# Performance work log

Measured on AMD Instinct MI355X. Metric: run time of the kernel, lower is better.

Reference implementation:

```python
import jax, jax.numpy as jnp
import numpy as np

TEMP = 16.0  # sqrt(in_dim=256), module default when temperature=None
BN_EPS = 1e-5


def setup_inputs() -> dict:
    key = jax.random.key(0)
    ks = jax.random.split(key, 8)
    B, Cin, T, H, W = 8, 256, 8, 16, 16
    FF, Cout = 512, 256
    # small init scale keeps softmax logits in a sane range
    s = 0.02
    return {
        "x": jax.random.normal(ks[0], (B, Cin, T, H, W), jnp.float32),
        "Wk": jax.random.normal(ks[1], (FF, Cin), jnp.float32) * s,
        "Wq": jax.random.normal(ks[2], (FF, Cin), jnp.float32) * s,
        "Wv": jax.random.normal(ks[3], (FF, Cin), jnp.float32) * s,
        "Wout": jax.random.normal(ks[4], (Cout, FF), jnp.float32) * s,
        "bout": jax.random.normal(ks[5], (Cout,), jnp.float32) * s,
        "gamma": jnp.ones((Cout,), jnp.float32),
        "beta": jnp.zeros((Cout,), jnp.float32),
    }


def reference(x, Wk, Wq, Wv, Wout, bout, gamma, beta):
    B, Cin, T, H, W = x.shape
    N = T * H * W
    xf = x.reshape(B, Cin, N)                      # 1x1x1 conv == per-position matmul
    K = jnp.einsum('fc,bcn->bfn', Wk, xf)
    Q = jnp.einsum('fc,bcn->bfn', Wq, xf)
    V = jnp.einsum('fc,bcn->bfn', Wv, xf)
    KQ = jnp.einsum('bfi,bfj->bij', K, Q)          # [B, N, N] = K^T Q
    attn = jax.nn.softmax(KQ / TEMP, axis=2)
    # torch: sum(V[:, :, :, None] * attn[:, None], dim=3)
    #      = V[b,c,i] * sum_j attn[b,i,j]  (no need to materialize B x C x N x N)
    agg = V * jnp.sum(attn, axis=2)[:, None, :]    # [B, FF, N]
    o = jnp.einsum('of,bfn->bon', Wout, agg) + bout[None, :, None]
    o = jax.nn.relu(o).reshape(B, -1, T, H, W)
    y = x + o                                      # residual (in_dim == out_dim)
    # BatchNorm3d, training mode (fresh module): batch stats over (B, T, H, W)
    mean = jnp.mean(y, axis=(0, 2, 3, 4), keepdims=True)
    var = jnp.var(y, axis=(0, 2, 3, 4), keepdims=True)
    g = gamma[None, :, None, None, None]
    b = beta[None, :, None, None, None]
    return g * (y - mean) * jax.lax.rsqrt(var + BN_EPS) + b
```

## Files before the change

### kernel.cpp

```cpp
#include <hip/hip_runtime.h>

typedef __attribute__((ext_vector_type(8))) short short8;
typedef __attribute__((ext_vector_type(4))) float floatx4;

#define B_    8
#define CIN   256
#define NSP   2048
#define FF    512
#define COUT  256
#define NTOT  (B_*COUT*NSP)

__device__ __forceinline__ unsigned short f2bf(float f) {
  unsigned int u = __float_as_uint(f);
  u += 0x7fffu + ((u >> 16) & 1u);
  return (unsigned short)(u >> 16);
}

__global__ __launch_bounds__(256) void k1_prep(
    const float* __restrict__ x, const float* __restrict__ Wv,
    const float* __restrict__ Wout,
    unsigned short* __restrict__ Mb, unsigned short* __restrict__ XT,
    float* __restrict__ stats)
{
  __shared__ float lds[64 * 65];
  const int tid = threadIdx.x;
  const int bx  = blockIdx.x;

  if (bx < 32) {
    if (bx == 0) { stats[tid] = 0.f; stats[256 + tid] = 0.f; }
    const int rbase = bx * 8;
    #pragma unroll
    for (int i = 0; i < 16; ++i) {
      int idx = i * 256 + tid;
      lds[idx] = Wout[(size_t)rbase * 512 + idx];
    }
    __syncthreads();
    float acc[8] = {0.f,0.f,0.f,0.f,0.f,0.f,0.f,0.f};
    #pragma unroll 8
    for (int f = 0; f < 512; ++f) {
      float w = Wv[(size_t)f * 256 + tid];
      #pragma unroll
      for (int j = 0; j < 8; ++j) acc[j] += lds[j * 512 + f] * w;
    }
    #pragma unroll
    for (int j = 0; j < 8; ++j)
      Mb[(size_t)(rbase + j) * 256 + tid] = f2bf(acc[j]);
  } else {
    const int idx = bx - 32;
    const int b   = idx >> 7;
    const int rem = idx & 127;
    const int n0  = (rem & 31) * 64;
    const int c0  = (rem >> 5) * 64;
    const float* xb = x + (size_t)b * CIN * NSP;
    const int n_l = tid & 63;
    const int c_l0 = tid >> 6;
    #pragma unroll
    for (int p = 0; p < 16; ++p) {
      int c_l = c_l0 + p * 4;
      lds[c_l * 65 + n_l] = xb[(size_t)(c0 + c_l) * NSP + n0 + n_l];
    }
    __syncthreads();
    const int cp   = tid & 31;
    const int n_l2 = tid >> 5;
    unsigned int* XT32 = (unsigned int*)XT;
    #pragma unroll
    for (int p = 0; p < 8; ++p) {
      int nn = n_l2 + p * 8;
      unsigned short lo = f2bf(lds[(2 * cp)     * 65 + nn]);
      unsigned short hi = f2bf(lds[(2 * cp + 1) * 65 + nn]);
      XT32[((size_t)b * NSP + n0 + nn) * 128 + (c0 >> 1) + cp] =
          (unsigned int)lo | ((unsigned int)hi << 16);
    }
  }
}

__global__ __launch_bounds__(256) void k2_gemm(
    const float* __restrict__ x, const unsigned short* __restrict__ Mb,
    const unsigned short* __restrict__ XT, const float* __restrict__ bout,
    unsigned short* __restrict__ ybf, float* __restrict__ stats)
{
  __shared__ float ls[128], lq[128];
  const int tid  = threadIdx.x;
  const int lane = tid & 63;
  const int wave = tid >> 6;
  const int b    = blockIdx.z;
  const int ocb  = blockIdx.y * 128;
  const int nb   = blockIdx.x * 128;
  const int wocb = ocb + (wave & 1) * 64;
  const int wnb  = nb + (wave >> 1) * 64;
  const int m16  = lane & 15;
  const int q    = lane >> 4;

  if (tid < 128) { ls[tid] = 0.f; lq[tid] = 0.f; }

  floatx4 acc[4][4];
  #pragma unroll
  for (int i = 0; i < 4; ++i)
    #pragma unroll
    for (int j = 0; j < 4; ++j)
      acc[i][j] = (floatx4){0.f, 0.f, 0.f, 0.f};

  const unsigned short* Abase = Mb + (size_t)(wocb + m16) * 256 + q * 8;
  const unsigned short* Bbase = XT + ((size_t)b * NSP + wnb + m16) * 256 + q * 8;

  #pragma unroll
  for (int kk = 0; kk < 8; ++kk) {
    short8 av[4], bv[4];
    #pragma unroll
    for (int t = 0; t < 4; ++t) {
      av[t] = *(const short8*)(Abase + (size_t)t * 16 * 256 + kk * 32);
      bv[t] = *(const short8*)(Bbase + (size_t)t * 16 * 256 + kk * 32);
    }
    #pragma unroll
    for (int i = 0; i < 4; ++i)
      #pragma unroll
      for (int j = 0; j < 4; ++j)
        acc[i][j] = __builtin_amdgcn_mfma_f32_16x16x32_bf16(av[i], bv[j], acc[i][j], 0, 0, 0);
  }

  __syncthreads();

  #pragma unroll
  for (int ti = 0; ti < 4; ++ti) {
    #pragma unroll
    for (int r = 0; r < 4; ++r) {
      const int oc = wocb + ti * 16 + q * 4 + r;
      const float bo = bout[oc];
      float s = 0.f, s2 = 0.f;
      #pragma unroll
      for (int tj = 0; tj < 4; ++tj) {
        const int n = wnb + tj * 16 + m16;
        float o = acc[ti][tj][r] + bo;
        o = fmaxf(o, 0.f);
        const size_t gidx = ((size_t)(b * COUT + oc)) * NSP + n;
        float y = x[gidx] + o;
        ybf[gidx] = f2bf(y);
        s += y;
        s2 += y * y;
      }
      #pragma unroll
      for (int d = 1; d < 16; d <<= 1) {
        s  += __shfl_xor(s, d, 64);
        s2 += __shfl_xor(s2, d, 64);
      }
      if (m16 == 0) {
        atomicAdd(&ls[oc - ocb], s);
        atomicAdd(&lq[oc - ocb], s2);
      }
    }
  }
  __syncthreads();
  if (tid < 128) {
    atomicAdd(&stats[ocb + tid], ls[tid]);
    atomicAdd(&stats[256 + ocb + tid], lq[tid]);
  }
}

__global__ void k3_finalize(const float* __restrict__ stats,
                            const float* __restrict__ gamma,
                            const float* __restrict__ beta,
                            float* __restrict__ scsh)
{
  const int c = threadIdx.x;
  const float inv_n = 1.f / 16384.f;
  float m = stats[c] * inv_n;
  float v = stats[256 + c] * inv_n - m * m;
  float inv = rsqrtf(v + 1e-5f);
  float sc = gamma[c] * inv;
  scsh[c] = sc;
  scsh[256 + c] = beta[c] - m * sc;
}

__global__ __launch_bounds__(256) void k4_norm(
    const unsigned short* __restrict__ ybf, const float* __restrict__ scsh,
    float* __restrict__ out)
{
  const size_t i = ((size_t)blockIdx.x * 256 + threadIdx.x) * 8;
  const int c = (int)((i >> 11) & 255);
  const float sc = scsh[c], sh = scsh[256 + c];
  const uint4 raw = *(const uint4*)(ybf + i);
  float4 o0, o1;
  o0.x = __uint_as_float(raw.x << 16)         * sc + sh;
  o0.y = __uint_as_float(raw.x & 0xffff0000u) * sc + sh;
  o0.z = __uint_as_float(raw.y << 16)         * sc + sh;
  o0.w = __uint_as_float(raw.y & 0xffff0000u) * sc + sh;
  o1.x = __uint_as_float(raw.z << 16)         * sc + sh;
  o1.y = __uint_as_float(raw.z & 0xffff0000u) * sc + sh;
  o1.z = __uint_as_float(raw.w << 16)         * sc + sh;
  o1.w = __uint_as_float(raw.w & 0xffff0000u) * sc + sh;
  *(float4*)(out + i)     = o0;
  *(float4*)(out + i + 4) = o1;
}

extern "C" void kernel_launch(void* const* d_in, const int* in_sizes, int n_in,
                              void* d_out, int out_size, void* d_ws, size_t ws_size,
                              hipStream_t stream) {
  const float* x     = (const float*)d_in[0];
  const float* Wv    = (const float*)d_in[3];
  const float* Wout  = (const float*)d_in[4];
  const float* bout  = (const float*)d_in[5];
  const float* gamma = (const float*)d_in[6];
  const float* beta  = (const float*)d_in[7];
  float* out = (float*)d_out;

  char* w = (char*)d_ws;
  unsigned short* Mb = (unsigned short*)w;
  unsigned short* XT = (unsigned short*)(w + 131072);
  unsigned short* yb = (unsigned short*)(w + 131072 + 8388608);
  float* stats = (float*)(w + 131072 + 8388608 + 8388608);
  float* scsh  = stats + 512;

  hipLaunchKernelGGL(k1_prep, dim3(32 + 1024), dim3(256), 0, stream,
                     x, Wv, Wout, Mb, XT, stats);
  hipLaunchKernelGGL(k2_gemm, dim3(16, 2, 8), dim3(256), 0, stream,
                     x, Mb, XT, bout, yb, stats);
  hipLaunchKernelGGL(k3_finalize, dim3(1), dim3(256), 0, stream,
                     stats, gamma, beta, scsh);
  hipLaunchKernelGGL(k4_norm, dim3(NTOT / (256 * 8)), dim3(256), 0, stream,
                     yb, scsh, out);
}
```

Measured before the change: 128.3 us.

## Fuse all four kernels into one cooperative kernel with grid syncs

Merges the prep, GEMM, BN-finalize and normalize kernels into one cooperative launch of 256 blocks. Grid-wide syncs separate the phases. The GEMM results stay in registers across the stats sync, so the bf16 intermediate y is never written to or read back from memory. This removes three launch gaps and a round trip of the full activation tensor. The cost is fewer blocks for the x transpose phase, since each block now loops over tiles, plus the overhead of two grid barriers.

```diff
diff --git a/kernel.cpp b/kernel.cpp
--- a/kernel.cpp
+++ b/kernel.cpp
@@ -1,4 +1,7 @@
 #include <hip/hip_runtime.h>
+#include <hip/hip_cooperative_groups.h>
+
+namespace cg = cooperative_groups;
 
 typedef __attribute__((ext_vector_type(8))) short short8;
 typedef __attribute__((ext_vector_type(4))) float floatx4;
@@ -8,7 +11,6 @@
 #define NSP   2048
 #define FF    512
 #define COUT  256
-#define NTOT  (B_*COUT*NSP)
 
 __device__ __forceinline__ unsigned short f2bf(float f) {
   unsigned int u = __float_as_uint(f);
@@ -16,82 +18,79 @@
   return (unsigned short)(u >> 16);
 }
 
-__global__ __launch_bounds__(256) void k1_prep(
+__global__ __launch_bounds__(256) void fused_all(
     const float* __restrict__ x, const float* __restrict__ Wv,
-    const float* __restrict__ Wout,
+    const float* __restrict__ Wout, const float* __restrict__ bout,
+    const float* __restrict__ gamma, const float* __restrict__ beta,
     unsigned short* __restrict__ Mb, unsigned short* __restrict__ XT,
-    float* __restrict__ stats)
+    float* __restrict__ stats, float* __restrict__ out)
 {
   __shared__ float lds[64 * 65];
-  const int tid = threadIdx.x;
-  const int bx  = blockIdx.x;
+  __shared__ float ls[128], lq[128];
+  const int tid  = threadIdx.x;
+  const int bx   = blockIdx.x;
+  const int lane = tid & 63;
+  const int wave = tid >> 6;
+  const int m16  = lane & 15;
+  const int q    = lane >> 4;
+
+  if (tid < 128) { ls[tid] = 0.f; lq[tid] = 0.f; }
 
   if (bx < 32) {
     if (bx == 0) { stats[tid] = 0.f; stats[256 + tid] = 0.f; }
     const int rbase = bx * 8;
     #pragma unroll
-    for (int i = 0; i < 16; ++i) {
-      int idx = i * 256 + tid;
-      lds[idx] = Wout[(size_t)rbase * 512 + idx];
-    }
+    for (int i = 0; i < 16; ++i)
+      lds[i * 256 + tid] = Wout[(size_t)rbase * 512 + i * 256 + tid];
     __syncthreads();
-    float acc[8] = {0.f,0.f,0.f,0.f,0.f,0.f,0.f,0.f};
+    float a8[8] = {0.f,0.f,0.f,0.f,0.f,0.f,0.f,0.f};
     #pragma unroll 8
     for (int f = 0; f < 512; ++f) {
       float w = Wv[(size_t)f * 256 + tid];
       #pragma unroll
-      for (int j = 0; j < 8; ++j) acc[j] += lds[j * 512 + f] * w;
+      for (int j = 0; j < 8; ++j) a8[j] += lds[j * 512 + f] * w;
     }
     #pragma unroll
     for (int j = 0; j < 8; ++j)
-      Mb[(size_t)(rbase + j) * 256 + tid] = f2bf(acc[j]);
+      Mb[(size_t)(rbase + j) * 256 + tid] = f2bf(a8[j]);
   } else {
-    const int idx = bx - 32;
-    const int b   = idx >> 7;
-    const int rem = idx & 127;
-    const int n0  = (rem & 31) * 64;
-    const int c0  = (rem >> 5) * 64;
-    const float* xb = x + (size_t)b * CIN * NSP;
-    const int n_l = tid & 63;
-    const int c_l0 = tid >> 6;
-    #pragma unroll
-    for (int p = 0; p < 16; ++p) {
-      int c_l = c_l0 + p * 4;
-      lds[c_l * 65 + n_l] = xb[(size_t)(c0 + c_l) * NSP + n0 + n_l];
-    }
-    __syncthreads();
-    const int cp   = tid & 31;
-    const int n_l2 = tid >> 5;
-    unsigned int* XT32 = (unsigned int*)XT;
-    #pragma unroll
-    for (int p = 0; p < 8; ++p) {
-      int nn = n_l2 + p * 8;
-      unsigned short lo = f2bf(lds[(2 * cp)     * 65 + nn]);
-      unsigned short hi = f2bf(lds[(2 * cp + 1) * 65 + nn]);
-      XT32[((size_t)b * NSP + n0 + nn) * 128 + (c0 >> 1) + cp] =
-          (unsigned int)lo | ((unsigned int)hi << 16);
-    }
-  }
-}
-
-__global__ __launch_bounds__(256) void k2_gemm(
-    const float* __restrict__ x, const unsigned short* __restrict__ Mb,
-    const unsigned short* __restrict__ XT, const float* __restrict__ bout,
-    unsigned short* __restrict__ ybf, float* __restrict__ stats)
-{
-  __shared__ float ls[128], lq[128];
-  const int tid  = threadIdx.x;
-  const int lane = tid & 63;
-  const int wave = tid >> 6;
-  const int b    = blockIdx.z;
-  const int ocb  = blockIdx.y * 128;
-  const int nb   = blockIdx.x * 128;
+    for (int t = bx - 32; t < 1024; t += 224) {
+      __syncthreads();
+      const int tb  = t >> 7;
+      const int rem = t & 127;
+      const int n0  = (rem & 31) * 64;
+      const int c0  = (rem >> 5) * 64;
+      const float* xb = x + (size_t)tb * CIN * NSP;
+      const int n_l  = tid & 63;
+      const int c_l0 = tid >> 6;
+      #pragma unroll
+      for (int p = 0; p < 16; ++p) {
+        int c_l = c_l0 + p * 4;
+        lds[c_l * 65 + n_l] = xb[(size_t)(c0 + c_l) * NSP + n0 + n_l];
+      }
+      __syncthreads();
+      const int cp   = tid & 31;
+      const int n_l2 = tid >> 5;
+      unsigned int* XT32 = (unsigned int*)XT;
+      #pragma unroll
+      for (int p = 0; p < 8; ++p) {
+        int nn = n_l2 + p * 8;
+        unsigned short lo = f2bf(lds[(2 * cp)     * 65 + nn]);
+        unsigned short hi = f2bf(lds[(2 * cp + 1) * 65 + nn]);
+        XT32[((size_t)tb * NSP + n0 + nn) * 128 + (c0 >> 1) + cp] =
+            (unsigned int)lo | ((unsigned int)hi << 16);
+      }
+    }
+  }
+
+  __threadfence();
+  cg::this_grid().sync();
+
+  const int b    = bx >> 5;
+  const int ocb  = ((bx >> 4) & 1) * 128;
+  const int nb   = (bx & 15) * 128;
   const int wocb = ocb + (wave & 1) * 64;
   const int wnb  = nb + (wave >> 1) * 64;
-  const int m16  = lane & 15;
-  const int q    = lane >> 4;
-
-  if (tid < 128) { ls[tid] = 0.f; lq[tid] = 0.f; }
 
   floatx4 acc[4][4];
   #pragma unroll
@@ -134,7 +133,7 @@
         o = fmaxf(o, 0.f);
         const size_t gidx = ((size_t)(b * COUT + oc)) * NSP + n;
         float y = x[gidx] + o;
-        ybf[gidx] = f2bf(y);
+        acc[ti][tj][r] = y;
         s += y;
         s2 += y * y;
       }
@@ -154,42 +153,38 @@
     atomicAdd(&stats[ocb + tid], ls[tid]);
     atomicAdd(&stats[256 + ocb + tid], lq[tid]);
   }
-}
-
-__global__ void k3_finalize(const float* __restrict__ stats,
-                            const float* __restrict__ gamma,
-                            const float* __restrict__ beta,
-                            float* __restrict__ scsh)
-{
-  const int c = threadIdx.x;
-  const float inv_n = 1.f / 16384.f;
-  float m = stats[c] * inv_n;
-  float v = stats[256 + c] * inv_n - m * m;
-  float inv = rsqrtf(v + 1e-5f);
-  float sc = gamma[c] * inv;
-  scsh[c] = sc;
-  scsh[256 + c] = beta[c] - m * sc;
-}
-
-__global__ __launch_bounds__(256) void k4_norm(
-    const unsigned short* __restrict__ ybf, const float* __restrict__ scsh,
-    float* __restrict__ out)
-{
-  const size_t i = ((size_t)blockIdx.x * 256 + threadIdx.x) * 8;
-  const int c = (int)((i >> 11) & 255);
-  const float sc = scsh[c], sh = scsh[256 + c];
-  const uint4 raw = *(const uint4*)(ybf + i);
-  float4 o0, o1;
-  o0.x = __uint_as_float(raw.x << 16)         * sc + sh;
-  o0.y = __uint_as_float(raw.x & 0xffff0000u) * sc + sh;
-  o0.z = __uint_as_float(raw.y << 16)         * sc + sh;
-  o0.w = __uint_as_float(raw.y & 0xffff0000u) * sc + sh;
-  o1.x = __uint_as_float(raw.z << 16)         * sc + sh;
-  o1.y = __uint_as_float(raw.z & 0xffff0000u) * sc + sh;
-  o1.z = __uint_as_float(raw.w << 16)         * sc + sh;
-  o1.w = __uint_as_float(raw.w & 0xffff0000u) * sc + sh;
-  *(float4*)(out + i)     = o0;
-  *(float4*)(out + i + 4) = o1;
+
+  __threadfence();
+  cg::this_grid().sync();
+
+  if (tid < 128) {
+    const int oc = ocb + tid;
+    const float inv_n = 1.f / 16384.f;
+    float m = stats[oc] * inv_n;
+    float v = stats[256 + oc] * inv_n - m * m;
+    float inv = rsqrtf(v + 1e-5f);
+    float sc = gamma[oc] * inv;
+    ls[tid] = sc;
+    lq[tid] = beta[oc] - m * sc;
+  }
+  __syncthreads();
+
+  #pragma unroll
+  for (int ti = 0; ti < 4; ++ti) {
+    #pragma unroll
+    for (int r = 0; r < 4; ++r) {
+      const int ocl = (wave & 1) * 64 + ti * 16 + q * 4 + r;
+      const int oc  = ocb + ocl;
+      const float sc = ls[ocl];
+      const float sh = lq[ocl];
+      #pragma unroll
+      for (int tj = 0; tj < 4; ++tj) {
+        const int n = wnb + tj * 16 + m16;
+        const size_t gidx = ((size_t)(b * COUT + oc)) * NSP + n;
+        out[gidx] = acc[ti][tj][r] * sc + sh;
+      }
+    }
+  }
 }
 
 extern "C" void kernel_launch(void* const* d_in, const int* in_sizes, int n_in,
@@ -206,16 +201,11 @@
   char* w = (char*)d_ws;
   unsigned short* Mb = (unsigned short*)w;
   unsigned short* XT = (unsigned short*)(w + 131072);
-  unsigned short* yb = (unsigned short*)(w + 131072 + 8388608);
-  float* stats = (float*)(w + 131072 + 8388608 + 8388608);
-  float* scsh  = stats + 512;
-
-  hipLaunchKernelGGL(k1_prep, dim3(32 + 1024), dim3(256), 0, stream,
-                     x, Wv, Wout, Mb, XT, stats);
-  hipLaunchKernelGGL(k2_gemm, dim3(16, 2, 8), dim3(256), 0, stream,
-                     x, Mb, XT, bout, yb, stats);
-  hipLaunchKernelGGL(k3_finalize, dim3(1), dim3(256), 0, stream,
-                     stats, gamma, beta, scsh);
-  hipLaunchKernelGGL(k4_norm, dim3(NTOT / (256 * 8)), dim3(256), 0, stream,
-                     yb, scsh, out);
+  float* stats = (float*)(w + 131072 + 8388608);
+
+  void* args[] = {(void*)&x, (void*)&Wv, (void*)&Wout, (void*)&bout,
+                  (void*)&gamma, (void*)&beta, (void*)&Mb, (void*)&XT,
+                  (void*)&stats, (void*)&out};
+  hipLaunchCooperativeKernel((const void*)fused_all, dim3(256), dim3(256),
+                             args, 0, stream);
 }
```

New measurement: 247.8 us. +93.2%, slower.

## Drop transposed bf16 x copy; read fp32 x directly in GEMM, fuse normalize in place

Applied to the files above, without the earlier changes.

Removes the separate transpose/convert pass that wrote a bf16 transposed copy of x. The GEMM now loads fp32 x directly with strided scalar loads and packs it to bf16 in registers. The intermediate bf16 y buffer is gone: the GEMM writes fp32 y straight into the output, and one normalize kernel (with the stats finalize folded in) rescales it in place. The Wv·Wout product is recomputed with one 1024-thread block per output row. Risks: uncoalesced strided x loads in the GEMM, halved per-wave N tile, and truncating-style rounding for x.

```diff
diff --git a/kernel.cpp b/kernel.cpp
--- a/kernel.cpp
+++ b/kernel.cpp
@@ -3,119 +3,103 @@
 typedef __attribute__((ext_vector_type(8))) short short8;
 typedef __attribute__((ext_vector_type(4))) float floatx4;
 
-#define B_    8
-#define CIN   256
-#define NSP   2048
-#define FF    512
-#define COUT  256
-#define NTOT  (B_*COUT*NSP)
+#define CIN  256
+#define NSP  2048
+#define COUT 256
 
-__device__ __forceinline__ unsigned short f2bf(float f) {
+__device__ __forceinline__ unsigned short f2bf_rne(float f) {
   unsigned int u = __float_as_uint(f);
   u += 0x7fffu + ((u >> 16) & 1u);
   return (unsigned short)(u >> 16);
 }
 
-__global__ __launch_bounds__(256) void k1_prep(
-    const float* __restrict__ x, const float* __restrict__ Wv,
-    const float* __restrict__ Wout,
-    unsigned short* __restrict__ Mb, unsigned short* __restrict__ XT,
-    float* __restrict__ stats)
+__device__ __forceinline__ unsigned int pack_bf16_hu(float lo, float hi) {
+  unsigned int a = __float_as_uint(lo) + 0x8000u;
+  unsigned int b = __float_as_uint(hi) + 0x8000u;
+  return __builtin_amdgcn_perm(b, a, 0x07060302u);
+}
+
+__global__ __launch_bounds__(1024) void k1_m(
+    const float* __restrict__ Wv, const float* __restrict__ Wout,
+    unsigned short* __restrict__ Mb, float* __restrict__ stats)
 {
-  __shared__ float lds[64 * 65];
+  __shared__ float ws[512];
+  __shared__ float red[4][256];
   const int tid = threadIdx.x;
-  const int bx  = blockIdx.x;
-
-  if (bx < 32) {
-    if (bx == 0) { stats[tid] = 0.f; stats[256 + tid] = 0.f; }
-    const int rbase = bx * 8;
-    #pragma unroll
-    for (int i = 0; i < 16; ++i) {
-      int idx = i * 256 + tid;
-      lds[idx] = Wout[(size_t)rbase * 512 + idx];
-    }
-    __syncthreads();
-    float acc[8] = {0.f,0.f,0.f,0.f,0.f,0.f,0.f,0.f};
-    #pragma unroll 8
-    for (int f = 0; f < 512; ++f) {
-      float w = Wv[(size_t)f * 256 + tid];
-      #pragma unroll
-      for (int j = 0; j < 8; ++j) acc[j] += lds[j * 512 + f] * w;
-    }
-    #pragma unroll
-    for (int j = 0; j < 8; ++j)
-      Mb[(size_t)(rbase + j) * 256 + tid] = f2bf(acc[j]);
-  } else {
-    const int idx = bx - 32;
-    const int b   = idx >> 7;
-    const int rem = idx & 127;
-    const int n0  = (rem & 31) * 64;
-    const int c0  = (rem >> 5) * 64;
-    const float* xb = x + (size_t)b * CIN * NSP;
-    const int n_l = tid & 63;
-    const int c_l0 = tid >> 6;
-    #pragma unroll
-    for (int p = 0; p < 16; ++p) {
-      int c_l = c_l0 + p * 4;
-      lds[c_l * 65 + n_l] = xb[(size_t)(c0 + c_l) * NSP + n0 + n_l];
-    }
-    __syncthreads();
-    const int cp   = tid & 31;
-    const int n_l2 = tid >> 5;
-    unsigned int* XT32 = (unsigned int*)XT;
-    #pragma unroll
-    for (int p = 0; p < 8; ++p) {
-      int nn = n_l2 + p * 8;
-      unsigned short lo = f2bf(lds[(2 * cp)     * 65 + nn]);
-      unsigned short hi = f2bf(lds[(2 * cp + 1) * 65 + nn]);
-      XT32[((size_t)b * NSP + n0 + nn) * 128 + (c0 >> 1) + cp] =
-          (unsigned int)lo | ((unsigned int)hi << 16);
-    }
+  const int r   = blockIdx.x;
+  if (r == 0 && tid < 512) stats[tid] = 0.f;
+  if (tid < 512) ws[tid] = Wout[(size_t)r * 512 + tid];
+  __syncthreads();
+  const int c  = tid & 255;
+  const int fs = tid >> 8;
+  float acc = 0.f;
+  #pragma unroll 16
+  for (int f0 = 0; f0 < 128; ++f0) {
+    int f = fs * 128 + f0;
+    acc += ws[f] * Wv[(size_t)f * 256 + c];
+  }
+  red[fs][c] = acc;
+  __syncthreads();
+  if (tid < 256) {
+    float s = red[0][tid] + red[1][tid] + red[2][tid] + red[3][tid];
+    Mb[(size_t)r * 256 + tid] = f2bf_rne(s);
   }
 }
 
 __global__ __launch_bounds__(256) void k2_gemm(
     const float* __restrict__ x, const unsigned short* __restrict__ Mb,
-    const unsigned short* __restrict__ XT, const float* __restrict__ bout,
-    unsigned short* __restrict__ ybf, float* __restrict__ stats)
+    const float* __restrict__ bout, float* __restrict__ stats,
+    float* __restrict__ out)
 {
   __shared__ float ls[128], lq[128];
   const int tid  = threadIdx.x;
   const int lane = tid & 63;
   const int wave = tid >> 6;
-  const int b    = blockIdx.z;
-  const int ocb  = blockIdx.y * 128;
-  const int nb   = blockIdx.x * 128;
-  const int wocb = ocb + (wave & 1) * 64;
-  const int wnb  = nb + (wave >> 1) * 64;
   const int m16  = lane & 15;
   const int q    = lane >> 4;
+  const int nb   = blockIdx.x * 64;
+  const int ocb  = blockIdx.y * 128;
+  const int b    = blockIdx.z;
+  const int wocb = ocb + (wave & 1) * 64;
+  const int wnb  = nb + (wave >> 1) * 32;
 
   if (tid < 128) { ls[tid] = 0.f; lq[tid] = 0.f; }
 
-  floatx4 acc[4][4];
+  floatx4 acc[4][2];
   #pragma unroll
   for (int i = 0; i < 4; ++i)
     #pragma unroll
-    for (int j = 0; j < 4; ++j)
+    for (int j = 0; j < 2; ++j)
       acc[i][j] = (floatx4){0.f, 0.f, 0.f, 0.f};
 
-  const unsigned short* Abase = Mb + (size_t)(wocb + m16) * 256 + q * 8;
-  const unsigned short* Bbase = XT + ((size_t)b * NSP + wnb + m16) * 256 + q * 8;
+  const unsigned short* Ab = Mb + (size_t)(wocb + m16) * 256 + q * 8;
+  const float* xb = x + (size_t)b * CIN * NSP;
+  const float* Bb = xb + (size_t)(q * 8) * NSP + wnb + m16;
 
   #pragma unroll
   for (int kk = 0; kk < 8; ++kk) {
-    short8 av[4], bv[4];
+    short8 av[4];
     #pragma unroll
-    for (int t = 0; t < 4; ++t) {
-      av[t] = *(const short8*)(Abase + (size_t)t * 16 * 256 + kk * 32);
-      bv[t] = *(const short8*)(Bbase + (size_t)t * 16 * 256 + kk * 32);
+    for (int ti = 0; ti < 4; ++ti)
+      av[ti] = *(const short8*)(Ab + (size_t)ti * 16 * 256 + kk * 32);
+    short8 bv[2];
+    #pragma unroll
+    for (int tj = 0; tj < 2; ++tj) {
+      const float* bp = Bb + (size_t)(kk * 32) * NSP + tj * 16;
+      union { unsigned int u[4]; short8 v; } p;
+      #pragma unroll
+      for (int j = 0; j < 4; ++j) {
+        float f0 = bp[(size_t)(2 * j) * NSP];
+        float f1 = bp[(size_t)(2 * j + 1) * NSP];
+        p.u[j] = pack_bf16_hu(f0, f1);
+      }
+      bv[tj] = p.v;
     }
     #pragma unroll
-    for (int i = 0; i < 4; ++i)
+    for (int ti = 0; ti < 4; ++ti)
       #pragma unroll
-      for (int j = 0; j < 4; ++j)
-        acc[i][j] = __builtin_amdgcn_mfma_f32_16x16x32_bf16(av[i], bv[j], acc[i][j], 0, 0, 0);
+      for (int tj = 0; tj < 2; ++tj)
+        acc[ti][tj] = __builtin_amdgcn_mfma_f32_16x16x32_bf16(av[ti], bv[tj], acc[ti][tj], 0, 0, 0);
   }
 
   __syncthreads();
@@ -124,17 +108,17 @@
   for (int ti = 0; ti < 4; ++ti) {
     #pragma unroll
     for (int r = 0; r < 4; ++r) {
-      const int oc = wocb + ti * 16 + q * 4 + r;
+      const int ocl = (wave & 1) * 64 + ti * 16 + q * 4 + r;
+      const int oc  = ocb + ocl;
       const float bo = bout[oc];
       float s = 0.f, s2 = 0.f;
       #pragma unroll
-      for (int tj = 0; tj < 4; ++tj) {
+      for (int tj = 0; tj < 2; ++tj) {
         const int n = wnb + tj * 16 + m16;
-        float o = acc[ti][tj][r] + bo;
-        o = fmaxf(o, 0.f);
         const size_t gidx = ((size_t)(b * COUT + oc)) * NSP + n;
+        float o = fmaxf(acc[ti][tj][r] + bo, 0.f);
         float y = x[gidx] + o;
-        ybf[gidx] = f2bf(y);
+        out[gidx] = y;
         s += y;
         s2 += y * y;
       }
@@ -144,8 +128,8 @@
         s2 += __shfl_xor(s2, d, 64);
       }
       if (m16 == 0) {
-        atomicAdd(&ls[oc - ocb], s);
-        atomicAdd(&lq[oc - ocb], s2);
+        atomicAdd(&ls[ocl], s);
+        atomicAdd(&lq[ocl], s2);
       }
     }
   }
@@ -156,40 +140,26 @@
   }
 }
 
-__global__ void k3_finalize(const float* __restrict__ stats,
-                            const float* __restrict__ gamma,
-                            const float* __restrict__ beta,
-                            float* __restrict__ scsh)
+__global__ __launch_bounds__(256) void k3_norm(
+    const float* __restrict__ stats, const float* __restrict__ gamma,
+    const float* __restrict__ beta, float* __restrict__ out)
 {
-  const int c = threadIdx.x;
+  const int row = blockIdx.x;
+  const int oc  = row & 255;
   const float inv_n = 1.f / 16384.f;
-  float m = stats[c] * inv_n;
-  float v = stats[256 + c] * inv_n - m * m;
-  float inv = rsqrtf(v + 1e-5f);
-  float sc = gamma[c] * inv;
-  scsh[c] = sc;
-  scsh[256 + c] = beta[c] - m * sc;
-}
-
-__global__ __launch_bounds__(256) void k4_norm(
-    const unsigned short* __restrict__ ybf, const float* __restrict__ scsh,
-    float* __restrict__ out)
-{
-  const size_t i = ((size_t)blockIdx.x * 256 + threadIdx.x) * 8;
-  const int c = (int)((i >> 11) & 255);
-  const float sc = scsh[c], sh = scsh[256 + c];
-  const uint4 raw = *(const uint4*)(ybf + i);
-  float4 o0, o1;
-  o0.x = __uint_as_float(raw.x << 16)         * sc + sh;
-  o0.y = __uint_as_float(raw.x & 0xffff0000u) * sc + sh;
-  o0.z = __uint_as_float(raw.y << 16)         * sc + sh;
-  o0.w = __uint_as_float(raw.y & 0xffff0000u) * sc + sh;
-  o1.x = __uint_as_float(raw.z << 16)         * sc + sh;
-  o1.y = __uint_as_float(raw.z & 0xffff0000u) * sc + sh;
-  o1.z = __uint_as_float(raw.w << 16)         * sc + sh;
-  o1.w = __uint_as_float(raw.w & 0xffff0000u) * sc + sh;
-  *(float4*)(out + i)     = o0;
-  *(float4*)(out + i + 4) = o1;
+  const float m  = stats[oc] * inv_n;
+  const float v  = stats[256 + oc] * inv_n - m * m;
+  const float sc = gamma[oc] * rsqrtf(v + 1e-5f);
+  const float sh = beta[oc] - m * sc;
+  float* p = out + (size_t)row * 2048 + threadIdx.x * 8;
+  float4 a = *(const float4*)p;
+  float4 c = *(const float4*)(p + 4);
+  a.x = a.x * sc + sh; a.y = a.y * sc + sh;
+  a.z = a.z * sc + sh; a.w = a.w * sc + sh;
+  c.x = c.x * sc + sh; c.y = c.y * sc + sh;
+  c.z = c.z * sc + sh; c.w = c.w * sc + sh;
+  *(float4*)p = a;
+  *(float4*)(p + 4) = c;
 }
 
 extern "C" void kernel_launch(void* const* d_in, const int* in_sizes, int n_in,
@@ -205,17 +175,12 @@
 
   char* w = (char*)d_ws;
   unsigned short* Mb = (unsigned short*)w;
-  unsigned short* XT = (unsigned short*)(w + 131072);
-  unsigned short* yb = (unsigned short*)(w + 131072 + 8388608);
-  float* stats = (float*)(w + 131072 + 8388608 + 8388608);
-  float* scsh  = stats + 512;
+  float* stats = (float*)(w + 131072);
 
-  hipLaunchKernelGGL(k1_prep, dim3(32 + 1024), dim3(256), 0, stream,
-                     x, Wv, Wout, Mb, XT, stats);
-  hipLaunchKernelGGL(k2_gemm, dim3(16, 2, 8), dim3(256), 0, stream,
-                     x, Mb, XT, bout, yb, stats);
-  hipLaunchKernelGGL(k3_finalize, dim3(1), dim3(256), 0, stream,
-                     stats, gamma, beta, scsh);
-  hipLaunchKernelGGL(k4_norm, dim3(NTOT / (256 * 8)), dim3(256), 0, stream,
-                     yb, scsh, out);
+  hipLaunchKernelGGL(k1_m,    dim3(256),       dim3(1024), 0, stream,
+                     Wv, Wout, Mb, stats);
+  hipLaunchKernelGGL(k2_gemm, dim3(32, 2, 8),  dim3(256),  0, stream,
+                     x, Mb, bout, stats, out);
+  hipLaunchKernelGGL(k3_norm, dim3(2048),      dim3(256),  0, stream,
+                     stats, gamma, beta, out);
 }
```

After: 114.0 us, median of 3. 11.1% less time.
